# Kernel optimization log

Measured on AMD Instinct MI355X. Metric: run time of the kernel, lower is better.

Reference implementation:

```python
import jax, jax.numpy as jnp
import numpy as np
import math

HID = 2048
NH = 8
KVH = 1
HD = 256
REP = NH // KVH
THETA = 10000.0
B, S = 2, 2048
NEG = -1e9  # additive mask value for disallowed positions


def setup_inputs() -> dict:
    key = jax.random.key(0)
    ks = jax.random.split(key, 6)
    x = jax.random.normal(ks[0], (B, S, HID), dtype=jnp.float32)
    # causal additive mask [B,1,S,S]
    causal = jnp.tril(jnp.ones((S, S), dtype=bool))
    attn_mask = jnp.where(causal, 0.0, NEG).astype(jnp.float32)[None, None]
    attn_mask = jnp.broadcast_to(attn_mask, (B, 1, S, S))
    pos_ids = jnp.broadcast_to(jnp.arange(S, dtype=jnp.int64 if jax.config.jax_enable_x64 else jnp.int32), (B, S))
    sc = 0.02
    wq = jax.random.normal(ks[1], (HID, NH * HD), dtype=jnp.float32) * sc
    wk = jax.random.normal(ks[2], (HID, KVH * HD), dtype=jnp.float32) * sc
    wv = jax.random.normal(ks[3], (HID, KVH * HD), dtype=jnp.float32) * sc
    wo = jax.random.normal(ks[4], (NH * HD, HID), dtype=jnp.float32) * sc
    return {"x": x, "attn_mask": attn_mask, "pos_ids": pos_ids,
            "wq": wq, "wk": wk, "wv": wv, "wo": wo}


def _rotate_half(t):
    h = t.shape[-1] // 2
    return jnp.concatenate([-t[..., h:], t[..., :h]], axis=-1)


def _rope_cos_sin(pos_ids, dtype):
    inv_freq = 1.0 / (THETA ** (jnp.arange(0, HD, 2, dtype=jnp.float32) / HD))  # [HD/2]
    freqs = pos_ids.astype(jnp.float32)[:, :, None] * inv_freq[None, None, :]  # [B,S,HD/2]
    emb = jnp.concatenate([freqs, freqs], axis=-1)                              # [B,S,HD]
    # unsqueeze head dim -> [B,1,S,HD]
    return jnp.cos(emb)[:, None].astype(dtype), jnp.sin(emb)[:, None].astype(dtype)


def reference(x, attn_mask, pos_ids, wq, wk, wv, wo):
    b, s, _ = x.shape
    q = (x @ wq).reshape(b, s, NH, HD).transpose(0, 2, 1, 3)    # [B,NH,S,HD]
    k = (x @ wk).reshape(b, s, KVH, HD).transpose(0, 2, 1, 3)   # [B,KVH,S,HD]
    v = (x @ wv).reshape(b, s, KVH, HD).transpose(0, 2, 1, 3)   # [B,KVH,S,HD]
    cos, sin = _rope_cos_sin(pos_ids, q.dtype)
    q = q * cos + _rotate_half(q) * sin
    k = k * cos + _rotate_half(k) * sin
    # GQA: group query heads over shared KV head instead of materializing repeat_kv
    qg = q.reshape(b, KVH, REP, s, HD)
    scores = jnp.einsum('bgrqd,bgkd->bgrqk', qg, k) / math.sqrt(HD)  # [B,KVH,REP,S,S]
    scores = scores.reshape(b, NH, s, s) + attn_mask
    attn = jax.nn.softmax(scores.astype(jnp.float32), axis=-1).astype(q.dtype)  # [B,NH,S,S]
    # dropout p=0.0 -> identity
    pg = attn.reshape(b, KVH, REP, s, s)
    out = jnp.einsum('bgrqk,bgkd->bgrqd', pg, v).reshape(b, NH, s, HD)
    out = out.transpose(0, 2, 1, 3).reshape(b, s, NH * HD) @ wo  # [B,S,HID]
    return out, attn
```

## Files before the change

### kernel.cpp

```cpp
#include <hip/hip_runtime.h>
#include <cstdint>
#include <cmath>

#define HID_ 2048
#define NH_ 8
#define HD_ 256
#define B_ 2
#define S_ 2048
#define BS_ (B_*S_)
#define QKVW_ 2560

typedef short short8 __attribute__((ext_vector_type(8)));
typedef float floatx4 __attribute__((ext_vector_type(4)));

static __device__ __forceinline__ unsigned short f2bf(float f) {
  union { float f; unsigned u; } v; v.f = f;
  return (unsigned short)((v.u + 0x7FFFu + ((v.u >> 16) & 1u)) >> 16);
}
static __device__ __forceinline__ float bf2f(unsigned short h) {
  union { unsigned u; float f; } v; v.u = ((unsigned)h) << 16;
  return v.f;
}

static __device__ __forceinline__ void gload_lds16(const void* g, void* l) {
  __builtin_amdgcn_global_load_lds(
      (const __attribute__((address_space(1))) unsigned int*)g,
      (__attribute__((address_space(3))) unsigned int*)l, 16, 0, 0);
}


__global__ void cast_f32_bf16_k(const float* __restrict__ in, unsigned short* __restrict__ out, long n) {
  long i = ((long)blockIdx.x * blockDim.x + threadIdx.x) * 4;
  if (i >= n) return;
  float4 v = *reinterpret_cast<const float4*>(in + i);
  ushort4 o; o.x = f2bf(v.x); o.y = f2bf(v.y); o.z = f2bf(v.z); o.w = f2bf(v.w);
  *reinterpret_cast<ushort4*>(out + i) = o;
}

__global__ void transpose_f2b_k(const float* __restrict__ in, unsigned short* __restrict__ out, int R, int C) {
  __shared__ float tile[32][33];
  int c0 = blockIdx.x * 32, r0 = blockIdx.y * 32;
  int tx = threadIdx.x, ty = threadIdx.y;
  #pragma unroll
  for (int i = 0; i < 4; i++)
    tile[ty + i*8][tx] = in[(long)(r0 + ty + i*8) * C + c0 + tx];
  __syncthreads();
  #pragma unroll
  for (int i = 0; i < 4; i++)
    out[(long)(c0 + ty + i*8) * R + r0 + tx] = f2bf(tile[tx][ty + i*8]);
}

__global__ void transpose_strided_k(const unsigned short* __restrict__ in, unsigned short* __restrict__ out,
                                    int ld_in, int ld_out, long in_bs, long out_bs) {
  __shared__ unsigned short tile[32][33];
  in += (long)blockIdx.z * in_bs; out += (long)blockIdx.z * out_bs;
  int c0 = blockIdx.x * 32, r0 = blockIdx.y * 32;
  int tx = threadIdx.x, ty = threadIdx.y;
  #pragma unroll
  for (int i = 0; i < 4; i++)
    tile[ty + i*8][tx] = in[(long)(r0 + ty + i*8) * ld_in + c0 + tx];
  __syncthreads();
  #pragma unroll
  for (int i = 0; i < 4; i++)
    out[(long)(c0 + ty + i*8) * ld_out + r0 + tx] = tile[tx][ty + i*8];
}

__global__ void rope_k(unsigned short* __restrict__ qk, const int* __restrict__ pos_ids,
                       int heads, int row_stride, long total) {
  long idx = (long)blockIdx.x * blockDim.x + threadIdx.x;
  if (idx >= total) return;
  int per_row = heads * (HD_/2);
  int r  = (int)(idx / per_row);
  int rem = (int)(idx % per_row);
  int h = rem / (HD_/2);
  int i = rem % (HD_/2);
  float posf = (float)pos_ids[r];
  float freq = expf(-(float)i * (logf(10000.0f) / 128.0f));
  float ang = posf * freq;
  float c = cosf(ang), s = sinf(ang);
  unsigned short* p = qk + (long)r * row_stride + (long)h * HD_;
  float a = bf2f(p[i]), b = bf2f(p[i + 128]);
  p[i]       = f2bf(a * c - b * s);
  p[i + 128] = f2bf(b * c + a * s);
}

template<int EPI>
__global__ __launch_bounds__(256)
void gemm_bt_k(const void* __restrict__ Av, const unsigned short* __restrict__ Bt,
               void* __restrict__ Cv, int K, long lda, long ldb, long ldc) {
  __shared__ unsigned short Al[128 * 32];
  __shared__ unsigned short Bl[128 * 32];

  int tid = threadIdx.x;
  int lane = tid & 63, wave = tid >> 6;
  int bm = blockIdx.y * 128, bn = blockIdx.x * 128;

  const unsigned short* Abase = (const unsigned short*)Av + (long)bm * lda;
  const unsigned short* Bbase = Bt + (long)bn * ldb;

  floatx4 zero = {0.f, 0.f, 0.f, 0.f};
  floatx4 acc[4][4];
  #pragma unroll
  for (int i = 0; i < 4; i++)
    #pragma unroll
    for (int j = 0; j < 4; j++) acc[i][j] = zero;

  const int wm = (wave >> 1) * 64, wn = (wave & 1) * 64;
  const int lr = lane & 15, lq = lane >> 4;

  for (int k0 = 0; k0 < K; k0 += 32) {
    #pragma unroll
    for (int c = 0; c < 2; c++) {
      int e = c * 2048 + tid * 8;
      int row = e >> 5, col = e & 31;
      gload_lds16(Abase + (long)row * lda + k0 + col, (char*)Al + c * 4096 + wave * 1024);
    }
    #pragma unroll
    for (int c = 0; c < 2; c++) {
      int e = c * 2048 + tid * 8;
      int row = e >> 5, col = e & 31;
      gload_lds16(Bbase + (long)row * ldb + k0 + col, (char*)Bl + c * 4096 + wave * 1024);
    }
    __syncthreads();

    short8 af[4], bfr[4];
    #pragma unroll
    for (int i = 0; i < 4; i++)
      af[i] = *reinterpret_cast<const short8*>(&Al[(wm + i*16 + lr) * 32 + lq * 8]);
    #pragma unroll
    for (int j = 0; j < 4; j++)
      bfr[j] = *reinterpret_cast<const short8*>(&Bl[(wn + j*16 + lr) * 32 + lq * 8]);
    #pragma unroll
    for (int i = 0; i < 4; i++)
      #pragma unroll
      for (int j = 0; j < 4; j++)
        acc[i][j] = __builtin_amdgcn_mfma_f32_16x16x32_bf16(af[i], bfr[j], acc[i][j], 0, 0, 0);
    __syncthreads();
  }

  if (EPI == 0) {
    unsigned short* C = (unsigned short*)Cv;
    #pragma unroll
    for (int i = 0; i < 4; i++)
      #pragma unroll
      for (int r = 0; r < 4; r++) {
        int row = bm + wm + i*16 + lq*4 + r;
        #pragma unroll
        for (int j = 0; j < 4; j++) {
          int col = bn + wn + j*16 + lr;
          C[(long)row * ldc + col] = f2bf(acc[i][j][r]);
        }
      }
  } else {
    float* C = (float*)Cv;
    #pragma unroll
    for (int i = 0; i < 4; i++)
      #pragma unroll
      for (int r = 0; r < 4; r++) {
        int row = bm + wm + i*16 + lq*4 + r;
        #pragma unroll
        for (int j = 0; j < 4; j++) {
          int col = bn + wn + j*16 + lr;
          C[(long)row * ldc + col] = acc[i][j][r];
        }
      }
  }
}

__global__ __launch_bounds__(256, 2)
void attn_fused_k(const unsigned short* __restrict__ qkv, const unsigned short* __restrict__ v_t,
                  float* __restrict__ attn, unsigned short* __restrict__ o_bf,
                  float* __restrict__ rowinv) {
  int z = blockIdx.x;
  int b = z >> 3, h = z & 7;
  int t = 31 - blockIdx.y;
  int bm = t * 64;
  int nkt = t / 2 + 1;

  const unsigned short* Qg = qkv + (long)b * S_ * QKVW_ + (long)h * HD_;
  const unsigned short* Kg = qkv + (long)b * S_ * QKVW_ + 2048;
  const unsigned short* Vt = v_t + (long)b * HD_ * S_;
  float* Az = attn + (long)z * S_ * S_;

  __shared__ unsigned short Kb[2][128 * 64];
  __shared__ unsigned short Vb[2][128 * 64];

  int tid = threadIdx.x;
  int lane = tid & 63, wave = tid >> 6;
  int lr = lane & 15, lq = lane >> 4;

  {
    int ce = nkt * 128;
    int perrow = (S_ - ce) >> 2;
    float4 zf = {0.f, 0.f, 0.f, 0.f};
    for (int i = tid; i < 64 * perrow; i += 256) {
      int r = i / perrow, c = i - r * perrow;
      *reinterpret_cast<float4*>(Az + (long)(bm + r) * S_ + ce + c * 4) = zf;
    }
  }

  short8 aq[8];
  {
    const unsigned short* qrow = Qg + (long)(bm + wave*16 + lr) * QKVW_;
    #pragma unroll
    for (int f = 0; f < 8; f++)
      aq[f] = *reinterpret_cast<const short8*>(qrow + f*32 + lq*8);
  }

  auto stageK = [&](int kt_, int c_) {
    char* dst = (char*)Kb[(kt_ + c_) & 1];
    const unsigned short* src = Kg + (long)(kt_ * 128) * QKVW_ + c_ * 64;
    #pragma unroll
    for (int cc = 0; cc < 4; cc++) {
      int q = cc * 256 + tid;
      int row = q >> 3, g = q & 7;
      gload_lds16(src + (long)row * QKVW_ + ((g ^ (row & 7)) << 3),
                  dst + cc * 4096 + wave * 1024);
    }
  };
  auto stageV = [&](int kt_, int p_) {
    int dh = p_ & 1, sh = p_ >> 1;
    char* dst = (char*)Vb[p_ & 1];
    const unsigned short* src = Vt + (long)(dh * 128) * S_ + kt_ * 128 + sh * 64;
    #pragma unroll
    for (int cc = 0; cc < 4; cc++) {
      int q = cc * 256 + tid;
      int row = q >> 3, g = q & 7;
      gload_lds16(src + (long)row * S_ + ((g ^ (row & 7)) << 3),
                  dst + cc * 4096 + wave * 1024);
    }
  };

  floatx4 zero = {0.f, 0.f, 0.f, 0.f};
  floatx4 oacc[16];
  #pragma unroll
  for (int j = 0; j < 16; j++) oacc[j] = zero;
  float rsum[4] = {0.f, 0.f, 0.f, 0.f};

  stageK(0, 0);
  __syncthreads();

  for (int kt = 0; kt < nkt; kt++) {
    int pb = kt & 1;
    floatx4 sacc[8];
    #pragma unroll
    for (int j = 0; j < 8; j++) sacc[j] = zero;

    #pragma unroll
    for (int c = 0; c < 4; c++) {
      if (c < 3) stageK(kt, c + 1);
      if (c == 2) stageV(kt, 0);
      if (c == 3) stageV(kt, 1);
      const unsigned short* Kc = Kb[(kt + c) & 1];
      #pragma unroll
      for (int kk = 0; kk < 2; kk++) {
        #pragma unroll
        for (int j = 0; j < 8; j++) {
          int R = j*16 + lr, G = kk*4 + lq;
          short8 bk = *reinterpret_cast<const short8*>(&Kc[R*64 + ((G ^ (R & 7)) << 3)]);
          sacc[j] = __builtin_amdgcn_mfma_f32_16x16x32_bf16(aq[c*2 + kk], bk, sacc[j], 0, 0, 0);
        }
      }
      __syncthreads();
    }

    unsigned short* Pl = Kb[pb];
    #pragma unroll
    for (int j = 0; j < 8; j++) {
      float v[4];
      #pragma unroll
      for (int r = 0; r < 4; r++) {
        int row_l = wave*16 + lq*4 + r;
        int col_g = kt*128 + j*16 + lr;
        float pv = (col_g <= bm + row_l) ? __expf(sacc[j][r] * 0.0625f) : 0.f;
        v[r] = pv;
        rsum[r] += pv;
        int Gw = j*2 + (lr >> 3);
        Pl[row_l*128 + ((Gw ^ (row_l & 7)) << 3) + (lr & 7)] = f2bf(pv);
      }
      float w[4];
      #pragma unroll
      for (int r = 0; r < 4; r++) w[r] = __shfl_xor(v[r], 1, 64);
      int colb = kt*128 + j*16 + (lr & ~1);
      if (!(lr & 1)) {
        #pragma unroll
        for (int r = 0; r < 2; r++) {
          int row = bm + wave*16 + lq*4 + r;
          float2 st; st.x = v[r]; st.y = w[r];
          *reinterpret_cast<float2*>(Az + (long)row * S_ + colb) = st;
        }
      } else {
        #pragma unroll
        for (int r = 2; r < 4; r++) {
          int row = bm + wave*16 + lq*4 + r;
          float2 st; st.x = w[r]; st.y = v[r];
          *reinterpret_cast<float2*>(Az + (long)row * S_ + colb) = st;
        }
      }
    }

    #pragma unroll
    for (int p = 0; p < 4; p++) {
      if (p == 0 && kt + 1 < nkt) stageK(kt + 1, 0);
      if (p == 1) stageV(kt, 2);
      if (p == 2) stageV(kt, 3);
      int dh = p & 1, sh = p >> 1;
      const unsigned short* Vc = Vb[p & 1];
      short8 ap[2];
      #pragma unroll
      for (int kk = 0; kk < 2; kk++) {
        int R = wave*16 + lr, G = sh*8 + kk*4 + lq;
        ap[kk] = *reinterpret_cast<const short8*>(&Pl[R*128 + ((G ^ (R & 7)) << 3)]);
      }
      #pragma unroll
      for (int kk = 0; kk < 2; kk++) {
        #pragma unroll
        for (int j2 = 0; j2 < 8; j2++) {
          int R = j2*16 + lr, G = kk*4 + lq;
          short8 bv = *reinterpret_cast<const short8*>(&Vc[R*64 + ((G ^ (R & 7)) << 3)]);
          oacc[dh*8 + j2] = __builtin_amdgcn_mfma_f32_16x16x32_bf16(ap[kk], bv, oacc[dh*8 + j2], 0, 0, 0);
        }
      }
      __syncthreads();
    }
  }

  #pragma unroll
  for (int r = 0; r < 4; r++) {
    float s = rsum[r];
    #pragma unroll
    for (int o = 1; o < 16; o <<= 1) s += __shfl_xor(s, o, 64);
    rsum[r] = 1.0f / s;
  }
  if (lr == 0) {
    #pragma unroll
    for (int r = 0; r < 4; r++)
      rowinv[(long)z * S_ + bm + wave*16 + lq*4 + r] = rsum[r];
  }

  unsigned short* C = o_bf + (long)b * S_ * HID_ + (long)h * HD_;
  #pragma unroll
  for (int dh = 0; dh < 2; dh++)
    #pragma unroll
    for (int j2 = 0; j2 < 8; j2++)
      #pragma unroll
      for (int r = 0; r < 4; r++) {
        int row = bm + wave*16 + lq*4 + r;
        int col = dh*128 + j2*16 + lr;
        C[(long)row * HID_ + col] = f2bf(oacc[dh*8 + j2][r] * rsum[r]);
      }
}

__global__ __launch_bounds__(256)
void attn_rescale_k(float* __restrict__ attn, const float* __restrict__ rowinv) {
  int z = blockIdx.y;
  int i = blockIdx.x;
  int m = (int)((sqrtf(8.f * (float)i + 1.f) - 1.f) * 0.5f);
  while ((m + 1) * (m + 2) / 2 <= i) m++;
  while (m * (m + 1) / 2 > i) m--;
  int n = i - m * (m + 1) / 2;

  int tid = threadIdx.x;
  int rr = tid >> 5, cc = tid & 31;
  float* base = attn + (long)z * S_ * S_ + (long)(m * 128) * S_ + n * 128;
  const float* invb = rowinv + (long)z * S_ + m * 128;
  #pragma unroll 4
  for (int it = 0; it < 16; it++) {
    int row = it * 8 + rr;
    float inv = invb[row];
    float4* p = reinterpret_cast<float4*>(base + (long)row * S_) + cc;
    float4 v = *p;
    v.x *= inv; v.y *= inv; v.z *= inv; v.w *= inv;
    *p = v;
  }
}


extern "C" void kernel_launch(void* const* d_in, const int* in_sizes, int n_in,
                              void* d_out, int out_size, void* d_ws, size_t ws_size,
                              hipStream_t stream) {
  (void)in_sizes; (void)n_in; (void)out_size; (void)ws_size;
  const float* x   = (const float*)d_in[0];
  const int*   pos = (const int*)d_in[2];
  const float* wq  = (const float*)d_in[3];
  const float* wk  = (const float*)d_in[4];
  const float* wv  = (const float*)d_in[5];
  const float* wo  = (const float*)d_in[6];
  float* out  = (float*)d_out;
  float* attn = out + (long)B_ * S_ * HID_;

  char* p = (char*)d_ws;
  auto take = [&](size_t n) { char* r = p; p += (n + 255) & ~(size_t)255; return r; };
  unsigned short* x_bf   = (unsigned short*)take((size_t)BS_ * HID_ * 2);
  unsigned short* wqkv_t = (unsigned short*)take((size_t)QKVW_ * HID_ * 2);
  unsigned short* wo_t   = (unsigned short*)take((size_t)HID_ * HID_ * 2);
  unsigned short* qkv    = (unsigned short*)take((size_t)BS_ * QKVW_ * 2);
  unsigned short* v_t    = (unsigned short*)take((size_t)B_ * HD_ * S_ * 2);
  unsigned short* o_bf   = (unsigned short*)take((size_t)BS_ * HID_ * 2);
  float*          rinv   = (float*)take((size_t)B_ * NH_ * S_ * 4);

  dim3 tb(32, 8);

  cast_f32_bf16_k<<<(BS_ * HID_) / 1024, 256, 0, stream>>>(x, x_bf, (long)BS_ * HID_);

  transpose_f2b_k<<<dim3(HID_/32, HID_/32), tb, 0, stream>>>(wq, wqkv_t, HID_, HID_);
  transpose_f2b_k<<<dim3(HD_/32,  HID_/32), tb, 0, stream>>>(wk, wqkv_t + (size_t)2048 * HID_, HID_, HD_);
  transpose_f2b_k<<<dim3(HD_/32,  HID_/32), tb, 0, stream>>>(wv, wqkv_t + (size_t)2304 * HID_, HID_, HD_);
  transpose_f2b_k<<<dim3(HID_/32, HID_/32), tb, 0, stream>>>(wo, wo_t, HID_, HID_);

  gemm_bt_k<0><<<dim3(QKVW_/128, BS_/128), 256, 0, stream>>>(
      x_bf, wqkv_t, qkv, HID_, HID_, HID_, QKVW_);

  rope_k<<<(BS_ * NH_ * (HD_/2)) / 256, 256, 0, stream>>>(
      qkv, pos, NH_, QKVW_, (long)BS_ * NH_ * (HD_/2));
  rope_k<<<(BS_ * (HD_/2)) / 256, 256, 0, stream>>>(
      qkv + 2048, pos, 1, QKVW_, (long)BS_ * (HD_/2));

  transpose_strided_k<<<dim3(HD_/32, S_/32, B_), tb, 0, stream>>>(
      qkv + 2304, v_t, QKVW_, S_, (long)S_ * QKVW_, (long)HD_ * S_);

  attn_fused_k<<<dim3(B_ * NH_, S_/64), 256, 0, stream>>>(qkv, v_t, attn, o_bf, rinv);

  attn_rescale_k<<<dim3(136, B_ * NH_), 256, 0, stream>>>(attn, rinv);

  gemm_bt_k<1><<<dim3(HID_/128, BS_/128), 256, 0, stream>>>(
      o_bf, wo_t, out, HID_, HID_, HID_, HID_);
}
```

Before: 694.4 us.

## Compute softmax row sums in a pre-pass and drop the attn rescale kernel

Adds a first pass over K in the fused attention kernel that recomputes QK^T only to accumulate exact softmax row sums. The second pass then writes already-normalized probabilities to attn and to the P tile for the PV product. This removes the separate rescale kernel, which re-read and re-wrote the causal half of the fp32 attention matrix, along with the rowinv buffer. The trade-off is doubling the QK^T MFMA work and K tile loads per block.

```diff
diff --git a/kernel.cpp b/kernel.cpp
--- a/kernel.cpp
+++ b/kernel.cpp
@@ -169,8 +169,7 @@
 
 __global__ __launch_bounds__(256, 2)
 void attn_fused_k(const unsigned short* __restrict__ qkv, const unsigned short* __restrict__ v_t,
-                  float* __restrict__ attn, unsigned short* __restrict__ o_bf,
-                  float* __restrict__ rowinv) {
+                  float* __restrict__ attn, unsigned short* __restrict__ o_bf) {
   int z = blockIdx.x;
   int b = z >> 3, h = z & 7;
   int t = 31 - blockIdx.y;
@@ -232,10 +231,53 @@
   };
 
   floatx4 zero = {0.f, 0.f, 0.f, 0.f};
+  float rsum[4] = {0.f, 0.f, 0.f, 0.f};
+
+  stageK(0, 0);
+  __syncthreads();
+  for (int kt = 0; kt < nkt; kt++) {
+    floatx4 sacc[8];
+    #pragma unroll
+    for (int j = 0; j < 8; j++) sacc[j] = zero;
+    #pragma unroll
+    for (int c = 0; c < 4; c++) {
+      if (c < 3) stageK(kt, c + 1);
+      const unsigned short* Kc = Kb[(kt + c) & 1];
+      #pragma unroll
+      for (int kk = 0; kk < 2; kk++) {
+        #pragma unroll
+        for (int j = 0; j < 8; j++) {
+          int R = j*16 + lr, G = kk*4 + lq;
+          short8 bk = *reinterpret_cast<const short8*>(&Kc[R*64 + ((G ^ (R & 7)) << 3)]);
+          sacc[j] = __builtin_amdgcn_mfma_f32_16x16x32_bf16(aq[c*2 + kk], bk, sacc[j], 0, 0, 0);
+        }
+      }
+      __syncthreads();
+    }
+    if (kt + 1 < nkt) stageK(kt + 1, 0);
+    #pragma unroll
+    for (int j = 0; j < 8; j++)
+      #pragma unroll
+      for (int r = 0; r < 4; r++) {
+        int row_l = wave*16 + lq*4 + r;
+        int col_g = kt*128 + j*16 + lr;
+        rsum[r] += (col_g <= bm + row_l) ? __expf(sacc[j][r] * 0.0625f) : 0.f;
+      }
+    __syncthreads();
+  }
+
+  float inv[4];
+  #pragma unroll
+  for (int r = 0; r < 4; r++) {
+    float s = rsum[r];
+    #pragma unroll
+    for (int o = 1; o < 16; o <<= 1) s += __shfl_xor(s, o, 64);
+    inv[r] = 1.0f / s;
+  }
+
   floatx4 oacc[16];
   #pragma unroll
   for (int j = 0; j < 16; j++) oacc[j] = zero;
-  float rsum[4] = {0.f, 0.f, 0.f, 0.f};
 
   stageK(0, 0);
   __syncthreads();
@@ -272,9 +314,8 @@
       for (int r = 0; r < 4; r++) {
         int row_l = wave*16 + lq*4 + r;
         int col_g = kt*128 + j*16 + lr;
-        float pv = (col_g <= bm + row_l) ? __expf(sacc[j][r] * 0.0625f) : 0.f;
+        float pv = (col_g <= bm + row_l) ? __expf(sacc[j][r] * 0.0625f) * inv[r] : 0.f;
         v[r] = pv;
-        rsum[r] += pv;
         int Gw = j*2 + (lr >> 3);
         Pl[row_l*128 + ((Gw ^ (row_l & 7)) << 3) + (lr & 7)] = f2bf(pv);
       }
@@ -325,19 +366,6 @@
     }
   }
 
-  #pragma unroll
-  for (int r = 0; r < 4; r++) {
-    float s = rsum[r];
-    #pragma unroll
-    for (int o = 1; o < 16; o <<= 1) s += __shfl_xor(s, o, 64);
-    rsum[r] = 1.0f / s;
-  }
-  if (lr == 0) {
-    #pragma unroll
-    for (int r = 0; r < 4; r++)
-      rowinv[(long)z * S_ + bm + wave*16 + lq*4 + r] = rsum[r];
-  }
-
   unsigned short* C = o_bf + (long)b * S_ * HID_ + (long)h * HD_;
   #pragma unroll
   for (int dh = 0; dh < 2; dh++)
@@ -347,32 +375,8 @@
       for (int r = 0; r < 4; r++) {
         int row = bm + wave*16 + lq*4 + r;
         int col = dh*128 + j2*16 + lr;
-        C[(long)row * HID_ + col] = f2bf(oacc[dh*8 + j2][r] * rsum[r]);
-      }
-}
-
-__global__ __launch_bounds__(256)
-void attn_rescale_k(float* __restrict__ attn, const float* __restrict__ rowinv) {
-  int z = blockIdx.y;
-  int i = blockIdx.x;
-  int m = (int)((sqrtf(8.f * (float)i + 1.f) - 1.f) * 0.5f);
-  while ((m + 1) * (m + 2) / 2 <= i) m++;
-  while (m * (m + 1) / 2 > i) m--;
-  int n = i - m * (m + 1) / 2;
-
-  int tid = threadIdx.x;
-  int rr = tid >> 5, cc = tid & 31;
-  float* base = attn + (long)z * S_ * S_ + (long)(m * 128) * S_ + n * 128;
-  const float* invb = rowinv + (long)z * S_ + m * 128;
-  #pragma unroll 4
-  for (int it = 0; it < 16; it++) {
-    int row = it * 8 + rr;
-    float inv = invb[row];
-    float4* p = reinterpret_cast<float4*>(base + (long)row * S_) + cc;
-    float4 v = *p;
-    v.x *= inv; v.y *= inv; v.z *= inv; v.w *= inv;
-    *p = v;
-  }
+        C[(long)row * HID_ + col] = f2bf(oacc[dh*8 + j2][r]);
+      }
 }
 
 
@@ -397,7 +401,6 @@
   unsigned short* qkv    = (unsigned short*)take((size_t)BS_ * QKVW_ * 2);
   unsigned short* v_t    = (unsigned short*)take((size_t)B_ * HD_ * S_ * 2);
   unsigned short* o_bf   = (unsigned short*)take((size_t)BS_ * HID_ * 2);
-  float*          rinv   = (float*)take((size_t)B_ * NH_ * S_ * 4);
 
   dim3 tb(32, 8);
 
@@ -419,9 +422,7 @@
   transpose_strided_k<<<dim3(HD_/32, S_/32, B_), tb, 0, stream>>>(
       qkv + 2304, v_t, QKVW_, S_, (long)S_ * QKVW_, (long)HD_ * S_);
 
-  attn_fused_k<<<dim3(B_ * NH_, S_/64), 256, 0, stream>>>(qkv, v_t, attn, o_bf, rinv);
-
-  attn_rescale_k<<<dim3(136, B_ * NH_), 256, 0, stream>>>(attn, rinv);
+  attn_fused_k<<<dim3(B_ * NH_, S_/64), 256, 0, stream>>>(qkv, v_t, attn, o_bf);
 
   gemm_bt_k<1><<<dim3(HID_/128, BS_/128), 256, 0, stream>>>(
       o_bf, wo_t, out, HID_, HID_, HID_, HID_);
```

Result: faster. 649.1 us (-6.5%).
